# Performance work log

Hardware: AMD Instinct MI355X
Metric: run time of the kernel (lower is better)

Reference implementation:

```python
import jax, jax.numpy as jnp
import numpy as np

IN_FEATURES = 512
OUT_FEATURES = 256
N = 2048

def setup_inputs() -> dict:
    key = jax.random.key(0)
    k1, k2, k3 = jax.random.split(key, 3)
    x = jax.random.normal(k1, (N, IN_FEATURES), dtype=jnp.float32)
    # kaiming_uniform_(a=sqrt(5)) -> uniform(-b, b) with b = sqrt(6/((1+5)*fan_in)) = 1/sqrt(fan_in)
    bound_w = 1.0 / np.sqrt(IN_FEATURES)
    weight = jax.random.uniform(k2, (OUT_FEATURES, IN_FEATURES), dtype=jnp.float32,
                                minval=-bound_w, maxval=bound_w)
    bound_b = 1.0 / np.sqrt(IN_FEATURES)
    bias = jax.random.uniform(k3, (OUT_FEATURES,), dtype=jnp.float32,
                              minval=-bound_b, maxval=bound_b)
    return {"x": x, "weight": weight, "bias": bias}

def reference(x, weight, bias):
    # MAM fully-connected (beta == 0 path):
    # prod[n, k, j] = x[n, k] * weight[j, k]
    # C[n, j] = max_k prod[n,k,j] + min_k prod[n,k,j] + bias[j]
    prod = x[:, :, None] * weight.T[None, :, :]   # [N, in, out]
    C = jnp.max(prod, axis=1) + jnp.min(prod, axis=1) + bias[None, :]
    return C
```

## Files before the change

kernel.cpp:

```cpp
#include <hip/hip_runtime.h>
#include <math.h>

#define N_ 2048
#define K_ 512
#define J_ 256
#define TN 64
#define TJ 32
#define BK 256
#define RP 260

typedef __attribute__((address_space(3))) float       lds_f;
typedef const __attribute__((address_space(1))) float glb_f;

__global__ __launch_bounds__(256) void mam_fused(
    const float* __restrict__ x, const float* __restrict__ w,
    const float* __restrict__ bias, float* __restrict__ out)
{
    __shared__ __align__(16) float xs[TN * RP];
    __shared__ __align__(16) float wsh[TJ * RP];

    const int t    = threadIdx.x;
    const int lane = t & 63;
    const int wid  = t >> 6;
    const int j0   = blockIdx.x * TJ;
    const int n0   = blockIdx.y * TN;
    const int tx   = t & 15;
    const int ty   = t >> 4;

    float mx[4][2], mn[4][2];
#pragma unroll
    for (int i = 0; i < 4; ++i)
#pragma unroll
        for (int j = 0; j < 2; ++j) {
            mx[i][j] = -__builtin_inff();
            mn[i][j] =  __builtin_inff();
        }

    for (int kc = 0; kc < K_; kc += BK) {
#pragma unroll
        for (int r = 0; r < 16; ++r) {
            const int row = wid * 16 + r;
            __builtin_amdgcn_global_load_lds(
                (glb_f*)(x + (size_t)(n0 + row) * K_ + kc + lane * 4),
                (lds_f*)(xs + row * RP), 16, 0, 0);
        }
#pragma unroll
        for (int r = 0; r < 8; ++r) {
            const int row = wid * 8 + r;
            __builtin_amdgcn_global_load_lds(
                (glb_f*)(w + (size_t)(j0 + row) * K_ + kc + lane * 4),
                (lds_f*)(wsh + row * RP), 16, 0, 0);
        }
        __syncthreads();

#pragma unroll 4
        for (int kk = 0; kk < BK; kk += 4) {
            float4 xv[4], wq[2];
#pragma unroll
            for (int i = 0; i < 4; ++i)
                xv[i] = *(const float4*)&xs[(ty * 4 + i) * RP + kk];
#pragma unroll
            for (int j = 0; j < 2; ++j)
                wq[j] = *(const float4*)&wsh[(tx * 2 + j) * RP + kk];
#pragma unroll
            for (int i = 0; i < 4; ++i) {
                const float xa[4] = {xv[i].x, xv[i].y, xv[i].z, xv[i].w};
#pragma unroll
                for (int j = 0; j < 2; ++j) {
                    const float wa[4] = {wq[j].x, wq[j].y, wq[j].z, wq[j].w};
#pragma unroll
                    for (int q = 0; q < 4; ++q) {
                        const float p = xa[q] * wa[q];
                        mx[i][j] = fmaxf(mx[i][j], p);
                        mn[i][j] = fminf(mn[i][j], p);
                    }
                }
            }
        }
        __syncthreads();
    }

    const float2 bi = *(const float2*)&bias[j0 + tx * 2];
#pragma unroll
    for (int i = 0; i < 4; ++i) {
        float2 o;
        o.x = mx[i][0] + mn[i][0] + bi.x;
        o.y = mx[i][1] + mn[i][1] + bi.y;
        *(float2*)&out[(size_t)(n0 + ty * 4 + i) * J_ + j0 + tx * 2] = o;
    }
}

extern "C" void kernel_launch(void* const* d_in, const int* in_sizes, int n_in,
                              void* d_out, int out_size, void* d_ws, size_t ws_size,
                              hipStream_t stream) {
    const float* x    = (const float*)d_in[0];
    const float* w    = (const float*)d_in[1];
    const float* bias = (const float*)d_in[2];
    float* out = (float*)d_out;

    dim3 grid(J_ / TJ, N_ / TN);
    mam_fused<<<grid, 256, 0, stream>>>(x, w, bias, out);
}
```

Before: 83.20 us.

## Hold weights in registers, split K across waves, use max3/min3 reductions

Restructures the kernel so each 512-thread block handles 8 rows and 128 output columns. Each of the 8 waves owns a 64-wide K slice and keeps its weight slice in registers, and x rows are staged in LDS. Partial max/min results are combined across waves through LDS, and inline v_max3/v_min3 instructions halve the reduction op count. The goal is to remove the per-k LDS weight reads and cut ALU instructions. The cost is heavy register use, since 32 float4 of weights per thread may limit occupancy, plus an extra LDS cross-wave reduction.

```diff
diff --git a/kernel.cpp b/kernel.cpp
--- a/kernel.cpp
+++ b/kernel.cpp
@@ -4,89 +4,105 @@
 #define N_ 2048
 #define K_ 512
 #define J_ 256
-#define TN 64
-#define TJ 32
-#define BK 256
-#define RP 260
 
 typedef __attribute__((address_space(3))) float       lds_f;
 typedef const __attribute__((address_space(1))) float glb_f;
 
-__global__ __launch_bounds__(256) void mam_fused(
+#define MAX3(acc, a, b) asm("v_max3_f32 %0, %0, %1, %2" : "+v"(acc) : "v"(a), "v"(b))
+#define MIN3(acc, a, b) asm("v_min3_f32 %0, %0, %1, %2" : "+v"(acc) : "v"(a), "v"(b))
+
+__global__ __launch_bounds__(512) void mam_fused6(
     const float* __restrict__ x, const float* __restrict__ w,
     const float* __restrict__ bias, float* __restrict__ out)
 {
-    __shared__ __align__(16) float xs[TN * RP];
-    __shared__ __align__(16) float wsh[TJ * RP];
+    __shared__ __align__(16) float xls[8 * 512];
+    __shared__ __align__(16) float cmb[8 * 8 * 128 * 2];
 
     const int t    = threadIdx.x;
     const int lane = t & 63;
-    const int wid  = t >> 6;
-    const int j0   = blockIdx.x * TJ;
-    const int n0   = blockIdx.y * TN;
-    const int tx   = t & 15;
-    const int ty   = t >> 4;
+    const int kc   = __builtin_amdgcn_readfirstlane(t >> 6);
 
-    float mx[4][2], mn[4][2];
+    const int wg0 = (int)blockIdx.x;
+    const int wg  = (wg0 & 7) * 64 + (wg0 >> 3);
+    const int jg  = wg & 1;
+    const int ng  = wg >> 1;
+
+    const int n0    = ng * 8;
+    const int jbase = jg * 128;
+
+    __builtin_amdgcn_global_load_lds(
+        (glb_f*)(x + (size_t)(n0 + kc) * K_ + lane * 4),
+        (lds_f*)(xls + kc * 512), 16, 0, 0);
+    __builtin_amdgcn_global_load_lds(
+        (glb_f*)(x + (size_t)(n0 + kc) * K_ + 256 + lane * 4),
+        (lds_f*)(xls + kc * 512 + 256), 16, 0, 0);
+
+    float4 wreg[2][16];
 #pragma unroll
-    for (int i = 0; i < 4; ++i)
+    for (int jj = 0; jj < 2; ++jj) {
+        const float4* wp =
+            (const float4*)(w + (size_t)(jbase + jj * 64 + lane) * K_ + kc * 64);
 #pragma unroll
-        for (int j = 0; j < 2; ++j) {
-            mx[i][j] = -__builtin_inff();
-            mn[i][j] =  __builtin_inff();
+        for (int g = 0; g < 16; ++g) wreg[jj][g] = wp[g];
+    }
+
+    __syncthreads();
+
+    float mx[8][2], mn[8][2];
+#pragma unroll
+    for (int n = 0; n < 8; ++n)
+#pragma unroll
+        for (int jj = 0; jj < 2; ++jj) {
+            mx[n][jj] = -__builtin_inff();
+            mn[n][jj] =  __builtin_inff();
         }
 
-    for (int kc = 0; kc < K_; kc += BK) {
 #pragma unroll
-        for (int r = 0; r < 16; ++r) {
-            const int row = wid * 16 + r;
-            __builtin_amdgcn_global_load_lds(
-                (glb_f*)(x + (size_t)(n0 + row) * K_ + kc + lane * 4),
-                (lds_f*)(xs + row * RP), 16, 0, 0);
-        }
+    for (int n = 0; n < 8; ++n) {
 #pragma unroll
-        for (int r = 0; r < 8; ++r) {
-            const int row = wid * 8 + r;
-            __builtin_amdgcn_global_load_lds(
-                (glb_f*)(w + (size_t)(j0 + row) * K_ + kc + lane * 4),
-                (lds_f*)(wsh + row * RP), 16, 0, 0);
-        }
-        __syncthreads();
-
-#pragma unroll 4
-        for (int kk = 0; kk < BK; kk += 4) {
-            float4 xv[4], wq[2];
+        for (int gb = 0; gb < 4; ++gb) {
+            float4 xv[4];
 #pragma unroll
-            for (int i = 0; i < 4; ++i)
-                xv[i] = *(const float4*)&xs[(ty * 4 + i) * RP + kk];
+            for (int g = 0; g < 4; ++g)
+                xv[g] = *(const float4*)&xls[n * 512 + kc * 64 + gb * 16 + g * 4];
 #pragma unroll
-            for (int j = 0; j < 2; ++j)
-                wq[j] = *(const float4*)&wsh[(tx * 2 + j) * RP + kk];
+            for (int g = 0; g < 4; ++g) {
 #pragma unroll
-            for (int i = 0; i < 4; ++i) {
-                const float xa[4] = {xv[i].x, xv[i].y, xv[i].z, xv[i].w};
-#pragma unroll
-                for (int j = 0; j < 2; ++j) {
-                    const float wa[4] = {wq[j].x, wq[j].y, wq[j].z, wq[j].w};
-#pragma unroll
-                    for (int q = 0; q < 4; ++q) {
-                        const float p = xa[q] * wa[q];
-                        mx[i][j] = fmaxf(mx[i][j], p);
-                        mn[i][j] = fminf(mn[i][j], p);
-                    }
+                for (int jj = 0; jj < 2; ++jj) {
+                    const float4 wv = wreg[jj][gb * 4 + g];
+                    const float p0 = xv[g].x * wv.x;
+                    const float p1 = xv[g].y * wv.y;
+                    const float p2 = xv[g].z * wv.z;
+                    const float p3 = xv[g].w * wv.w;
+                    MAX3(mx[n][jj], p0, p1); MAX3(mx[n][jj], p2, p3);
+                    MIN3(mn[n][jj], p0, p1); MIN3(mn[n][jj], p2, p3);
                 }
             }
         }
-        __syncthreads();
     }
 
-    const float2 bi = *(const float2*)&bias[j0 + tx * 2];
 #pragma unroll
-    for (int i = 0; i < 4; ++i) {
-        float2 o;
-        o.x = mx[i][0] + mn[i][0] + bi.x;
-        o.y = mx[i][1] + mn[i][1] + bi.y;
-        *(float2*)&out[(size_t)(n0 + ty * 4 + i) * J_ + j0 + tx * 2] = o;
+    for (int n = 0; n < 8; ++n)
+#pragma unroll
+        for (int jj = 0; jj < 2; ++jj) {
+            float2 v; v.x = mx[n][jj]; v.y = mn[n][jj];
+            *(float2*)&cmb[((kc * 8 + n) * 128 + jj * 64 + lane) * 2] = v;
+        }
+    __syncthreads();
+
+#pragma unroll
+    for (int i = 0; i < 2; ++i) {
+        const int u    = t + i * 512;
+        const int n    = u >> 7;
+        const int jcol = u & 127;
+        float a = -__builtin_inff(), b = __builtin_inff();
+#pragma unroll
+        for (int c = 0; c < 8; ++c) {
+            const float2 p = *(const float2*)&cmb[((c * 8 + n) * 128 + jcol) * 2];
+            a = fmaxf(a, p.x);
+            b = fminf(b, p.y);
+        }
+        out[(size_t)(n0 + n) * J_ + jbase + jcol] = a + b + bias[jbase + jcol];
     }
 }
 
@@ -98,6 +114,6 @@
     const float* bias = (const float*)d_in[2];
     float* out = (float*)d_out;
 
-    dim3 grid(J_ / TJ, N_ / TN);
-    mam_fused<<<grid, 256, 0, stream>>>(x, w, bias, out);
+    dim3 grid(512);
+    mam_fused6<<<grid, 512, 0, stream>>>(x, w, bias, out);
 }
```

Result: slower. 86.71 us (+4.2%).
